# Optimization experiments

Hardware: AMD Instinct MI355X
Metric: run time of the kernel (lower is better)

Reference implementation:

```python
import math
import jax, jax.numpy as jnp
import numpy as np

D = 1024        # latent_dim
H = 16          # num latent heads
HD = D // H     # head dim = 64
T_EMB = 9       # max(diffusion_steps+1, 2)
CLIP = 1.0      # latent_update_clip
LN_EPS = 1e-5


def layer_norm(x, g, b):
    m = jnp.mean(x, axis=-1, keepdims=True)
    v = jnp.mean(jnp.square(x - m), axis=-1, keepdims=True)
    return (x - m) * jax.lax.rsqrt(v + LN_EPS) * g + b


def setup_inputs() -> dict:
    key = jax.random.key(0)
    ks = jax.random.split(key, 10)
    B, S = 64, 64
    s = 0.02
    return {
        "latents": jax.random.normal(ks[0], (B, S, D), jnp.float32),
        "t_table": jax.random.normal(ks[1], (T_EMB, D), jnp.float32) * s,
        "attn_g": jnp.ones((D,), jnp.float32),
        "attn_b": jnp.zeros((D,), jnp.float32),
        "ffn_g": jnp.ones((D,), jnp.float32),
        "ffn_b": jnp.zeros((D,), jnp.float32),
        "Wq": jax.random.normal(ks[2], (D, D), jnp.float32) * s,
        "Wk": jax.random.normal(ks[3], (D, D), jnp.float32) * s,
        "Wv": jax.random.normal(ks[4], (D, D), jnp.float32) * s,
        "Wo": jax.random.normal(ks[5], (D, D), jnp.float32) * s,
        "Win": jax.random.normal(ks[6], (2 * D, D), jnp.float32) * s,
        "b_in": jnp.zeros((2 * D,), jnp.float32),
        "Wout": jax.random.normal(ks[7], (D, 2 * D), jnp.float32) * s,
        "b_out": jnp.zeros((D,), jnp.float32),
        "steps": 8,
    }


def _slot_attention(x, Wq, Wk, Wv, Wo):
    B, S, _ = x.shape
    scale = 1.0 / math.sqrt(HD)
    # torch Linear: y = x @ W.T ; weights stored (out, in)
    q = (x @ Wq.T).reshape(B, S, H, HD)
    k = (x @ Wk.T).reshape(B, S, H, HD)
    v = (x @ Wv.T).reshape(B, S, H, HD)
    scores = jnp.einsum("bqhd,bkhd->bhqk", q, k) * scale
    probs = jax.nn.softmax(scores, axis=-1)
    out = jnp.einsum("bhqk,bkhd->bqhd", probs, v).reshape(B, S, D)
    return out @ Wo.T


def reference(latents, t_table, attn_g, attn_b, ffn_g, ffn_b,
              Wq, Wk, Wv, Wo, Win, b_in, Wout, b_out, steps):
    h = latents
    for step in range(steps):
        step_id = min(step, T_EMB - 1)
        t_emb = t_table[step_id][None, None, :]          # [1,1,D]
        attn_update = _slot_attention(layer_norm(h + t_emb, attn_g, attn_b),
                                      Wq, Wk, Wv, Wo)
        ffn_in = layer_norm(h + t_emb + attn_update, ffn_g, ffn_b)
        ffn_update = jax.nn.silu(ffn_in @ Win.T + b_in) @ Wout.T + b_out
        update = attn_update + ffn_update
        unorm = jnp.maximum(jnp.linalg.norm(update, axis=-1, keepdims=True), 1e-6)
        update = update * jnp.minimum(CLIP / unorm, 1.0)
        h = h + update / steps
    return h
```

## Files before the change

### kernel.cpp

```cpp
#include <hip/hip_runtime.h>
#include <hip/hip_bf16.h>

typedef __attribute__((ext_vector_type(8))) short bf16x8;
typedef __attribute__((ext_vector_type(4))) float f32x4;
typedef __attribute__((ext_vector_type(4))) int i32x4;

static __device__ __forceinline__ short f2bf(float f) {
    __hip_bfloat16 h = __float2bfloat16(f);
    return __builtin_bit_cast(short, h);
}

static __device__ __forceinline__ void gload_lds16(const short* g, short* l) {
    __builtin_amdgcn_global_load_lds((const __attribute__((address_space(1))) void*)g,
                                     (__attribute__((address_space(3))) void*)l, 16, 0, 0);
}

__global__ void convert_kernel(const float* __restrict__ src, short* __restrict__ dst, int n) {
    for (int i = blockIdx.x * blockDim.x + threadIdx.x; i < n; i += gridDim.x * blockDim.x)
        dst[i] = f2bf(src[i]);
}

__global__ void copy_kernel(const float* __restrict__ src, float* __restrict__ dst, int n) {
    for (int i = blockIdx.x * blockDim.x + threadIdx.x; i < n; i += gridDim.x * blockDim.x)
        dst[i] = src[i];
}

__global__ __launch_bounds__(256) void ln_kernel(
    const float* __restrict__ hsrc, const float* __restrict__ trow,
    const float* __restrict__ add,
    const float* __restrict__ g, const float* __restrict__ bb,
    short* __restrict__ out)
{
    const int row = blockIdx.x;
    const int tid = threadIdx.x;
    const int lane = tid & 63;
    const int wid = tid >> 6;
    __shared__ float red[4];
    const float* hr = hsrc + (size_t)row * 1024;
    float x[4];
    float s = 0.f;
    #pragma unroll
    for (int i = 0; i < 4; ++i) {
        int c = tid + i * 256;
        float v = hr[c] + trow[c];
        if (add) v += add[(size_t)row * 1024 + c];
        x[i] = v; s += v;
    }
    #pragma unroll
    for (int o = 32; o >= 1; o >>= 1) s += __shfl_xor(s, o, 64);
    if (lane == 0) red[wid] = s;
    __syncthreads();
    float mean = (red[0] + red[1] + red[2] + red[3]) * (1.0f / 1024.0f);
    __syncthreads();
    float s2 = 0.f;
    #pragma unroll
    for (int i = 0; i < 4; ++i) { float d = x[i] - mean; s2 += d * d; }
    #pragma unroll
    for (int o = 32; o >= 1; o >>= 1) s2 += __shfl_xor(s2, o, 64);
    if (lane == 0) red[wid] = s2;
    __syncthreads();
    float var = (red[0] + red[1] + red[2] + red[3]) * (1.0f / 1024.0f);
    float rstd = rsqrtf(var + 1e-5f);
    #pragma unroll
    for (int i = 0; i < 4; ++i) {
        int c = tid + i * 256;
        out[(size_t)row * 1024 + c] = f2bf((x[i] - mean) * rstd * g[c] + bb[c]);
    }
}

template<int BM, int ACT, int ADD, int BIAS, int OUT_BF16>
__global__ __launch_bounds__(256) void gemm_kernel(
    const short* __restrict__ A, const short* __restrict__ B,
    const float* __restrict__ bias, const float* __restrict__ addsrc,
    void* __restrict__ Cout, int M, int N, int K)
{
    const int bn = blockIdx.x * 128;
    const int bm = blockIdx.y * BM;
    __shared__ __align__(16) short As[BM * 64];
    __shared__ __align__(16) short Bs[128 * 64];
    const int tid = threadIdx.x;
    const int lane = tid & 63;
    const int wid = tid >> 6;
    const int l15 = lane & 15;
    const int l4 = lane >> 4;

    constexpr int NF = (BM == 128) ? 4 : 2;
    const int rowbase = (BM == 128) ? (wid >> 1) * 64 : 0;
    const int colbase = (BM == 128) ? (wid & 1) * 64 : wid * 32;

    f32x4 acc[4][NF];
    #pragma unroll
    for (int m = 0; m < 4; ++m)
        #pragma unroll
        for (int n = 0; n < NF; ++n)
            acc[m][n] = (f32x4)(0.f);

    for (int k0 = 0; k0 < K; k0 += 64) {
        __syncthreads();
        #pragma unroll
        for (int i = 0; i < BM / 32; ++i) {
            int slot = i * 256 + tid;
            int row = slot >> 3;
            int colb = (slot & 7) * 16;
            int swz = (row & 7) << 4;
            const short* g = A + (size_t)(bm + row) * K + k0 + ((colb ^ swz) >> 1);
            gload_lds16(g, (short*)((char*)As + slot * 16));
        }
        #pragma unroll
        for (int i = 0; i < 4; ++i) {
            int slot = i * 256 + tid;
            int row = slot >> 3;
            int colb = (slot & 7) * 16;
            int swz = (row & 7) << 4;
            const short* g = B + (size_t)(bn + row) * K + k0 + ((colb ^ swz) >> 1);
            gload_lds16(g, (short*)((char*)Bs + slot * 16));
        }
        __syncthreads();
        #pragma unroll
        for (int ks = 0; ks < 2; ++ks) {
            int kb = ks * 64 + l4 * 16;
            bf16x8 a[4], b[NF];
            #pragma unroll
            for (int m = 0; m < 4; ++m) {
                int row = rowbase + m * 16 + l15;
                a[m] = *(const bf16x8*)((const char*)As + row * 128 + (kb ^ ((row & 7) << 4)));
            }
            #pragma unroll
            for (int n = 0; n < NF; ++n) {
                int row = colbase + n * 16 + l15;
                b[n] = *(const bf16x8*)((const char*)Bs + row * 128 + (kb ^ ((row & 7) << 4)));
            }
            #pragma unroll
            for (int m = 0; m < 4; ++m)
                #pragma unroll
                for (int n = 0; n < NF; ++n)
                    acc[m][n] = __builtin_amdgcn_mfma_f32_16x16x32_bf16(a[m], b[n], acc[m][n], 0, 0, 0);
        }
    }

    #pragma unroll
    for (int m = 0; m < 4; ++m) {
        int row = bm + rowbase + m * 16 + l4 * 4;
        #pragma unroll
        for (int n = 0; n < NF; ++n) {
            int col = bn + colbase + n * 16 + l15;
            float bv = BIAS ? bias[col] : 0.f;
            #pragma unroll
            for (int r = 0; r < 4; ++r) {
                float v = acc[m][n][r] + bv;
                if (ACT) v = v / (1.f + __expf(-v));
                if (ADD) v += addsrc[(size_t)(row + r) * N + col];
                if (OUT_BF16) ((short*)Cout)[(size_t)(row + r) * N + col] = f2bf(v);
                else          ((float*)Cout)[(size_t)(row + r) * N + col] = v;
            }
        }
    }
}

__global__ __launch_bounds__(256) void attn_kernel(
    const short* __restrict__ qkv,
    short* __restrict__ ctx)
{
    const int blk = blockIdx.x;
    const int b = blk >> 4, hh = blk & 15;
    const int bs0 = b * 64;
    __shared__ __align__(16) short qs[64 * 64];
    __shared__ __align__(16) short ks_[64 * 64];
    __shared__ __align__(16) short vt[64 * 64];
    __shared__ __align__(16) short ps[64 * 64];
    const int tid = threadIdx.x;
    const int lane = tid & 63;
    const int wid = tid >> 6;
    const int l15 = lane & 15;
    const int l4 = lane >> 4;

    #pragma unroll
    for (int i = 0; i < 2; ++i) {
        int slot = i * 256 + tid;
        int row = slot >> 3;
        int colb = (slot & 7) * 16;
        int swz = (row & 7) << 4;
        const short* gq = qkv + (size_t)(bs0 + row) * 3072 + hh * 64 + (slot & 7) * 8;
        *(i32x4*)((char*)qs + row * 128 + (colb ^ swz)) = *(const i32x4*)gq;
        const short* gk = qkv + (size_t)(bs0 + row) * 3072 + 1024 + hh * 64 + (slot & 7) * 8;
        *(i32x4*)((char*)ks_ + row * 128 + (colb ^ swz)) = *(const i32x4*)gk;
        const short* gv = qkv + (size_t)(bs0 + row) * 3072 + 2048 + hh * 64 + (slot & 7) * 8;
        i32x4 vv = *(const i32x4*)gv;
        const short* ve = (const short*)&vv;
        #pragma unroll
        for (int j = 0; j < 8; ++j) {
            int d = (slot & 7) * 8 + j;
            *(short*)((char*)vt + d * 128 + ((row * 2) ^ ((d & 7) << 4))) = ve[j];
        }
    }
    __syncthreads();

    f32x4 sc[4];
    #pragma unroll
    for (int n = 0; n < 4; ++n) sc[n] = (f32x4)(0.f);
    #pragma unroll
    for (int ksz = 0; ksz < 2; ++ksz) {
        int kb = ksz * 64 + l4 * 16;
        int arow = wid * 16 + l15;
        bf16x8 af = *(const bf16x8*)((const char*)qs + arow * 128 + (kb ^ ((arow & 7) << 4)));
        #pragma unroll
        for (int n = 0; n < 4; ++n) {
            int brow = n * 16 + l15;
            bf16x8 bf = *(const bf16x8*)((const char*)ks_ + brow * 128 + (kb ^ ((brow & 7) << 4)));
            sc[n] = __builtin_amdgcn_mfma_f32_16x16x32_bf16(af, bf, sc[n], 0, 0, 0);
        }
    }
    float sm[4];
    #pragma unroll
    for (int r = 0; r < 4; ++r) {
        float m = -1e30f;
        #pragma unroll
        for (int n = 0; n < 4; ++n) { sc[n][r] *= 0.125f; m = fmaxf(m, sc[n][r]); }
        #pragma unroll
        for (int o = 1; o < 16; o <<= 1) m = fmaxf(m, __shfl_xor(m, o, 64));
        float s = 0.f;
        #pragma unroll
        for (int n = 0; n < 4; ++n) { sc[n][r] = __expf(sc[n][r] - m); s += sc[n][r]; }
        #pragma unroll
        for (int o = 1; o < 16; o <<= 1) s += __shfl_xor(s, o, 64);
        sm[r] = 1.f / s;
    }
    #pragma unroll
    for (int n = 0; n < 4; ++n)
        #pragma unroll
        for (int r = 0; r < 4; ++r) {
            int row = wid * 16 + l4 * 4 + r;
            int col = n * 16 + l15;
            *(short*)((char*)ps + row * 128 + ((col * 2) ^ ((row & 7) << 4))) = f2bf(sc[n][r] * sm[r]);
        }
    __syncthreads();

    f32x4 o[4];
    #pragma unroll
    for (int n = 0; n < 4; ++n) o[n] = (f32x4)(0.f);
    #pragma unroll
    for (int ksz = 0; ksz < 2; ++ksz) {
        int kb = ksz * 64 + l4 * 16;
        int arow = wid * 16 + l15;
        bf16x8 af = *(const bf16x8*)((const char*)ps + arow * 128 + (kb ^ ((arow & 7) << 4)));
        #pragma unroll
        for (int n = 0; n < 4; ++n) {
            int vrow = n * 16 + l15;
            bf16x8 bf = *(const bf16x8*)((const char*)vt + vrow * 128 + (kb ^ ((vrow & 7) << 4)));
            o[n] = __builtin_amdgcn_mfma_f32_16x16x32_bf16(af, bf, o[n], 0, 0, 0);
        }
    }
    #pragma unroll
    for (int n = 0; n < 4; ++n)
        #pragma unroll
        for (int r = 0; r < 4; ++r) {
            int row = wid * 16 + l4 * 4 + r;
            int col = n * 16 + l15;
            ctx[(size_t)(bs0 + row) * 1024 + hh * 64 + col] = f2bf(o[n][r]);
        }
}

__global__ __launch_bounds__(256) void clip_kernel(const float* __restrict__ upd, float* __restrict__ h) {
    const int row = blockIdx.x;
    const int tid = threadIdx.x;
    const int lane = tid & 63;
    const int wid = tid >> 6;
    __shared__ float red[4];
    const float* ur = upd + (size_t)row * 1024;
    float x[4];
    float s = 0.f;
    #pragma unroll
    for (int i = 0; i < 4; ++i) { x[i] = ur[tid + i * 256]; s += x[i] * x[i]; }
    #pragma unroll
    for (int o = 32; o >= 1; o >>= 1) s += __shfl_xor(s, o, 64);
    if (lane == 0) red[wid] = s;
    __syncthreads();
    float nrm = sqrtf(red[0] + red[1] + red[2] + red[3]);
    float unorm = fmaxf(nrm, 1e-6f);
    float scale = fminf(1.0f / unorm, 1.0f) * 0.125f;
    #pragma unroll
    for (int i = 0; i < 4; ++i) {
        int c = tid + i * 256;
        h[(size_t)row * 1024 + c] += x[i] * scale;
    }
}

extern "C" void kernel_launch(void* const* d_in, const int* in_sizes, int n_in,
                              void* d_out, int out_size, void* d_ws, size_t ws_size,
                              hipStream_t stream) {
    const float* latents = (const float*)d_in[0];
    const float* t_table = (const float*)d_in[1];
    const float* attn_g  = (const float*)d_in[2];
    const float* attn_b  = (const float*)d_in[3];
    const float* ffn_g   = (const float*)d_in[4];
    const float* ffn_b   = (const float*)d_in[5];
    const float* Wq      = (const float*)d_in[6];
    const float* Wk      = (const float*)d_in[7];
    const float* Wv      = (const float*)d_in[8];
    const float* Wo      = (const float*)d_in[9];
    const float* Win     = (const float*)d_in[10];
    const float* b_in    = (const float*)d_in[11];
    const float* Wout    = (const float*)d_in[12];
    const float* b_out   = (const float*)d_in[13];

    char* ws = (char*)d_ws;
    size_t off = 0;
    auto alloc = [&](size_t bytes) { char* p = ws + off; off += (bytes + 255) & ~(size_t)255; return p; };
    short* wQKV = (short*)alloc((size_t)3072 * 1024 * 2);
    short* wO   = (short*)alloc((size_t)1024 * 1024 * 2);
    short* wIn  = (short*)alloc((size_t)2048 * 1024 * 2);
    short* wOut = (short*)alloc((size_t)1024 * 2048 * 2);
    short* xln  = (short*)alloc((size_t)4096 * 1024 * 2);
    short* qkv  = (short*)alloc((size_t)4096 * 3072 * 2);
    short* hidden = qkv;
    short* ctx  = (short*)alloc((size_t)4096 * 1024 * 2);
    float* au   = (float*)alloc((size_t)4096 * 1024 * 4);
    float* upd  = (float*)alloc((size_t)4096 * 1024 * 4);

    float* h = (float*)d_out;

    convert_kernel<<<1024, 256, 0, stream>>>(Wq,   wQKV,               1024 * 1024);
    convert_kernel<<<1024, 256, 0, stream>>>(Wk,   wQKV + 1024 * 1024, 1024 * 1024);
    convert_kernel<<<1024, 256, 0, stream>>>(Wv,   wQKV + 2048 * 1024, 1024 * 1024);
    convert_kernel<<<1024, 256, 0, stream>>>(Wo,   wO,                 1024 * 1024);
    convert_kernel<<<2048, 256, 0, stream>>>(Win,  wIn,                2048 * 1024);
    convert_kernel<<<2048, 256, 0, stream>>>(Wout, wOut,               2048 * 1024);
    copy_kernel<<<2048, 256, 0, stream>>>(latents, h, 4096 * 1024);

    for (int step = 0; step < 8; ++step) {
        const float* trow = t_table + (size_t)step * 1024;
        ln_kernel<<<4096, 256, 0, stream>>>(h, trow, nullptr, attn_g, attn_b, xln);
        gemm_kernel<128, 0, 0, 0, 1><<<dim3(24, 32), 256, 0, stream>>>(xln, wQKV, nullptr, nullptr, qkv, 4096, 3072, 1024);
        attn_kernel<<<1024, 256, 0, stream>>>(qkv, ctx);
        gemm_kernel<64, 0, 0, 0, 0><<<dim3(8, 64), 256, 0, stream>>>(ctx, wO, nullptr, nullptr, au, 4096, 1024, 1024);
        ln_kernel<<<4096, 256, 0, stream>>>(h, trow, au, ffn_g, ffn_b, xln);
        gemm_kernel<128, 1, 0, 1, 1><<<dim3(16, 32), 256, 0, stream>>>(xln, wIn, b_in, nullptr, hidden, 4096, 2048, 1024);
        gemm_kernel<64, 0, 1, 1, 0><<<dim3(8, 64), 256, 0, stream>>>(hidden, wOut, b_out, au, upd, 4096, 1024, 2048);
        clip_kernel<<<4096, 256, 0, stream>>>(upd, h);
    }
}
```

Baseline: 1.198 ms.

## Double-buffer GEMM LDS tiles and fuse clip with next-step attention LayerNorm

The GEMM kernel now uses two LDS buffers per operand. It issues the next K-tile's global-to-LDS loads before computing the current tile, with explicit vmcnt waits and barriers, so memory latency overlaps MFMA work. The per-step clip kernel is also fused with the following step's attention LayerNorm, removing one kernel launch and one full read of h per step. The cost is twice the LDS footprint, which may lower occupancy, and hand-written waitcnt counts that must match the number of loads issued.

```diff
diff --git a/kernel.cpp b/kernel.cpp
--- a/kernel.cpp
+++ b/kernel.cpp
@@ -68,6 +68,60 @@
     }
 }
 
+__global__ __launch_bounds__(256) void clipln_kernel(
+    const float* __restrict__ upd, float* __restrict__ h,
+    const float* __restrict__ trow,
+    const float* __restrict__ g, const float* __restrict__ bb,
+    short* __restrict__ out)
+{
+    const int row = blockIdx.x;
+    const int tid = threadIdx.x;
+    const int lane = tid & 63;
+    const int wid = tid >> 6;
+    __shared__ float red[4];
+    const float* ur = upd + (size_t)row * 1024;
+    float u[4], hn[4];
+    float s = 0.f;
+    #pragma unroll
+    for (int i = 0; i < 4; ++i) { u[i] = ur[tid + i * 256]; s += u[i] * u[i]; }
+    #pragma unroll
+    for (int o = 32; o >= 1; o >>= 1) s += __shfl_xor(s, o, 64);
+    if (lane == 0) red[wid] = s;
+    __syncthreads();
+    float nrm = sqrtf(red[0] + red[1] + red[2] + red[3]);
+    float scale = fminf(1.0f / fmaxf(nrm, 1e-6f), 1.0f) * 0.125f;
+    __syncthreads();
+    float sm = 0.f;
+    #pragma unroll
+    for (int i = 0; i < 4; ++i) {
+        int c = tid + i * 256;
+        hn[i] = h[(size_t)row * 1024 + c] + u[i] * scale;
+        h[(size_t)row * 1024 + c] = hn[i];
+        hn[i] += trow[c];
+        sm += hn[i];
+    }
+    #pragma unroll
+    for (int o = 32; o >= 1; o >>= 1) sm += __shfl_xor(sm, o, 64);
+    if (lane == 0) red[wid] = sm;
+    __syncthreads();
+    float mean = (red[0] + red[1] + red[2] + red[3]) * (1.0f / 1024.0f);
+    __syncthreads();
+    float s2 = 0.f;
+    #pragma unroll
+    for (int i = 0; i < 4; ++i) { float d = hn[i] - mean; s2 += d * d; }
+    #pragma unroll
+    for (int o = 32; o >= 1; o >>= 1) s2 += __shfl_xor(s2, o, 64);
+    if (lane == 0) red[wid] = s2;
+    __syncthreads();
+    float var = (red[0] + red[1] + red[2] + red[3]) * (1.0f / 1024.0f);
+    float rstd = rsqrtf(var + 1e-5f);
+    #pragma unroll
+    for (int i = 0; i < 4; ++i) {
+        int c = tid + i * 256;
+        out[(size_t)row * 1024 + c] = f2bf((hn[i] - mean) * rstd * g[c] + bb[c]);
+    }
+}
+
 template<int BM, int ACT, int ADD, int BIAS, int OUT_BF16>
 __global__ __launch_bounds__(256) void gemm_kernel(
     const short* __restrict__ A, const short* __restrict__ B,
@@ -76,14 +130,16 @@
 {
     const int bn = blockIdx.x * 128;
     const int bm = blockIdx.y * BM;
-    __shared__ __align__(16) short As[BM * 64];
-    __shared__ __align__(16) short Bs[128 * 64];
+    __shared__ __align__(16) short As[2][BM * 64];
+    __shared__ __align__(16) short Bs[2][128 * 64];
     const int tid = threadIdx.x;
     const int lane = tid & 63;
     const int wid = tid >> 6;
     const int l15 = lane & 15;
     const int l4 = lane >> 4;
 
+    constexpr int ALOADS = BM / 32;
+    constexpr int LOADS = ALOADS + 4;
     constexpr int NF = (BM == 128) ? 4 : 2;
     const int rowbase = (BM == 128) ? (wid >> 1) * 64 : 0;
     const int colbase = (BM == 128) ? (wid & 1) * 64 : wid * 32;
@@ -95,16 +151,15 @@
         for (int n = 0; n < NF; ++n)
             acc[m][n] = (f32x4)(0.f);
 
-    for (int k0 = 0; k0 < K; k0 += 64) {
-        __syncthreads();
-        #pragma unroll
-        for (int i = 0; i < BM / 32; ++i) {
+    auto stage = [&](int k0, int buf) {
+        #pragma unroll
+        for (int i = 0; i < ALOADS; ++i) {
             int slot = i * 256 + tid;
             int row = slot >> 3;
             int colb = (slot & 7) * 16;
             int swz = (row & 7) << 4;
             const short* g = A + (size_t)(bm + row) * K + k0 + ((colb ^ swz) >> 1);
-            gload_lds16(g, (short*)((char*)As + slot * 16));
+            gload_lds16(g, (short*)((char*)As[buf] + slot * 16));
         }
         #pragma unroll
         for (int i = 0; i < 4; ++i) {
@@ -113,9 +168,22 @@
             int colb = (slot & 7) * 16;
             int swz = (row & 7) << 4;
             const short* g = B + (size_t)(bn + row) * K + k0 + ((colb ^ swz) >> 1);
-            gload_lds16(g, (short*)((char*)Bs + slot * 16));
-        }
-        __syncthreads();
+            gload_lds16(g, (short*)((char*)Bs[buf] + slot * 16));
+        }
+    };
+
+    stage(0, 0);
+    const int nt = K >> 6;
+    for (int t = 0; t < nt; ++t) {
+        const int cur = t & 1;
+        if (t + 1 < nt) {
+            stage((t + 1) << 6, cur ^ 1);
+            if constexpr (LOADS == 8) asm volatile("s_waitcnt vmcnt(8)" ::: "memory");
+            else                      asm volatile("s_waitcnt vmcnt(6)" ::: "memory");
+        } else {
+            asm volatile("s_waitcnt vmcnt(0)" ::: "memory");
+        }
+        __builtin_amdgcn_s_barrier();
         #pragma unroll
         for (int ks = 0; ks < 2; ++ks) {
             int kb = ks * 64 + l4 * 16;
@@ -123,12 +191,12 @@
             #pragma unroll
             for (int m = 0; m < 4; ++m) {
                 int row = rowbase + m * 16 + l15;
-                a[m] = *(const bf16x8*)((const char*)As + row * 128 + (kb ^ ((row & 7) << 4)));
+                a[m] = *(const bf16x8*)((const char*)As[cur] + row * 128 + (kb ^ ((row & 7) << 4)));
             }
             #pragma unroll
             for (int n = 0; n < NF; ++n) {
                 int row = colbase + n * 16 + l15;
-                b[n] = *(const bf16x8*)((const char*)Bs + row * 128 + (kb ^ ((row & 7) << 4)));
+                b[n] = *(const bf16x8*)((const char*)Bs[cur] + row * 128 + (kb ^ ((row & 7) << 4)));
             }
             #pragma unroll
             for (int m = 0; m < 4; ++m)
@@ -136,6 +204,7 @@
                 for (int n = 0; n < NF; ++n)
                     acc[m][n] = __builtin_amdgcn_mfma_f32_16x16x32_bf16(a[m], b[n], acc[m][n], 0, 0, 0);
         }
+        __builtin_amdgcn_s_barrier();
     }
 
     #pragma unroll
@@ -327,15 +396,21 @@
     convert_kernel<<<2048, 256, 0, stream>>>(Wout, wOut,               2048 * 1024);
     copy_kernel<<<2048, 256, 0, stream>>>(latents, h, 4096 * 1024);
 
+    ln_kernel<<<4096, 256, 0, stream>>>(h, t_table, nullptr, attn_g, attn_b, xln);
+
     for (int step = 0; step < 8; ++step) {
         const float* trow = t_table + (size_t)step * 1024;
-        ln_kernel<<<4096, 256, 0, stream>>>(h, trow, nullptr, attn_g, attn_b, xln);
         gemm_kernel<128, 0, 0, 0, 1><<<dim3(24, 32), 256, 0, stream>>>(xln, wQKV, nullptr, nullptr, qkv, 4096, 3072, 1024);
         attn_kernel<<<1024, 256, 0, stream>>>(qkv, ctx);
         gemm_kernel<64, 0, 0, 0, 0><<<dim3(8, 64), 256, 0, stream>>>(ctx, wO, nullptr, nullptr, au, 4096, 1024, 1024);
         ln_kernel<<<4096, 256, 0, stream>>>(h, trow, au, ffn_g, ffn_b, xln);
         gemm_kernel<128, 1, 0, 1, 1><<<dim3(16, 32), 256, 0, stream>>>(xln, wIn, b_in, nullptr, hidden, 4096, 2048, 1024);
         gemm_kernel<64, 0, 1, 1, 0><<<dim3(8, 64), 256, 0, stream>>>(hidden, wOut, b_out, au, upd, 4096, 1024, 2048);
-        clip_kernel<<<4096, 256, 0, stream>>>(upd, h);
-    }
-}
+        if (step < 7) {
+            clipln_kernel<<<4096, 256, 0, stream>>>(upd, h, t_table + (size_t)(step + 1) * 1024,
+                                                    attn_g, attn_b, xln);
+        } else {
+            clip_kernel<<<4096, 256, 0, stream>>>(upd, h);
+        }
+    }
+}
```

After: 1.170 ms. 1.02x faster.
